# Optimization experiments

Hardware: AMD Instinct MI355X
Metric: run time of the kernel (lower is better)

Reference implementation:

```python
import jax, jax.numpy as jnp
import numpy as np

N, E, D = 50000, 1600000, 128


def _mk_w(key, shape):
    return jax.random.normal(key, shape, dtype=jnp.float32) * 0.05


def setup_inputs() -> dict:
    key = jax.random.key(0)
    ks = jax.random.split(key, 32)
    inp = {
        'x_in': jax.random.normal(ks[0], (N, D), dtype=jnp.float32),
        'rows': jax.random.randint(ks[1], (E,), 0, N, dtype=jnp.int64 if jax.config.jax_enable_x64 else jnp.int32),
        'cols': jax.random.randint(ks[2], (E,), 0, N, dtype=jnp.int64 if jax.config.jax_enable_x64 else jnp.int32),
        'vals': jax.random.uniform(ks[3], (E,), dtype=jnp.float32),
    }
    names = ['m1_W1', 'm1_W2', 'm2_W1', 'm2_W2', 'Wu1', 'Wu2', 'Wr1', 'Wr2', 'Wo1', 'Wo2']
    for i, n in enumerate(names):
        inp[n] = _mk_w(ks[4 + i], (D, D))
        inp[n.replace('W', 'b')] = jnp.zeros((D,), dtype=jnp.float32)
    return inp


def _mlp2(x, W1, b1, W2, b2):
    # 2-layer MLP: Linear -> ReLU -> Linear
    return jax.nn.relu(x @ W1 + b1) @ W2 + b2


def reference(x_in, rows, cols, vals,
              m1_W1, m1_b1, m1_W2, m1_b2,
              m2_W1, m2_b1, m2_W2, m2_b2,
              Wu1, bu1, Wu2, bu2,
              Wr1, br1, Wr2, br2,
              Wo1, bo1, Wo2, bo2):
    x = _mlp2(x_in, m1_W1, m1_b1, m1_W2, m1_b2)            # [N, D]
    # sparse COO spmm: out[i] = sum_e vals[e] * x[cols[e]] for rows[e] == i
    msgs = vals[:, None] * x[cols]                          # [E, D]
    agg = jax.ops.segment_sum(msgs, rows, num_segments=N)   # [N, D]
    out = _mlp2(agg, m2_W1, m2_b1, m2_W2, m2_b2)
    z = jax.nn.sigmoid(out @ Wu1 + bu1 + x @ Wu2 + bu2)
    r = jax.nn.sigmoid(out @ Wr1 + br1 + x @ Wr2 + br2)
    h = jnp.tanh(out @ Wo1 + bo1 + (r * x) @ Wo2 + bo2)
    return (1.0 - z) * x + z * h
```

## Files before the change

kernel.cpp:

```cpp
#include <hip/hip_runtime.h>

#define DD 128
#define BSHIFT 7
#define BROWS 128
#define MS_TILE 4096
#define MS_EPT 8
#define STAGE_CAP 6144

typedef __attribute__((ext_vector_type(8))) short short8;
typedef __attribute__((ext_vector_type(4))) float f32x4;
typedef unsigned short u16;
typedef unsigned int u32;

__device__ __forceinline__ u16 f2bf(float f) {
  u32 u = __builtin_bit_cast(u32, f);
  u += 0x7fffu + ((u >> 16) & 1u);
  return (u16)(u >> 16);
}
__device__ __forceinline__ float bf2f(u16 s) {
  u32 u = ((u32)s) << 16;
  return __builtin_bit_cast(float, u);
}
__device__ __forceinline__ float f16val(u32 cv) {
  return (float)__builtin_bit_cast(_Float16, (u16)(cv & 0xffffu));
}
__device__ __forceinline__ float sigmoidf_(float v) { return 1.f / (1.f + __expf(-v)); }
__device__ __forceinline__ float tanhf_(float v) {
  float e = __expf(-2.f * v);
  return (1.f - e) / (1.f + e);
}

struct WPtrs { const float* w[10]; };

__global__ void pack_weights(WPtrs wp, u16* __restrict__ bp) {
  const float* W = wp.w[blockIdx.x];
  u16* out = bp + (size_t)blockIdx.x * 16384;
  for (int o = threadIdx.x; o < 16384; o += blockDim.x) {
    int e = o & 7, lane = (o >> 3) & 63, nt = (o >> 9) & 7, ks = o >> 12;
    int k = ks * 32 + (lane >> 4) * 8 + e;
    int c = (lane & 15) + nt * 16;
    out[o] = f2bf(W[k * DD + c]);
  }
}

__global__ __launch_bounds__(512) void multisplit(const int* __restrict__ rows,
                                                  const int* __restrict__ cols,
                                                  const float* __restrict__ vals,
                                                  int* __restrict__ cursor,
                                                  uint2* __restrict__ recs,
                                                  int E, int NB, int cap) {
  __shared__ u32 hist[512];
  __shared__ u32 scan_tmp[512];
  __shared__ u32 hbase[512];
  __shared__ int gbase[512];
  __shared__ u32 rankc[512];
  __shared__ uint2 stage[MS_TILE];
  const int t = threadIdx.x;
  const int tile0 = blockIdx.x * MS_TILE;
  hist[t] = 0;
  rankc[t] = 0;
  __syncthreads();
  int myb[MS_EPT];
  u32 mycv[MS_EPT], myrow[MS_EPT];
#pragma unroll
  for (int j = 0; j < MS_EPT; ++j) {
    int e = tile0 + j * 512 + t;
    if (e < E) {
      int r = rows[e];
      int b = r >> BSHIFT;
      myb[j] = b;
      myrow[j] = (u32)r;
      _Float16 hf = (_Float16)vals[e];
      mycv[j] = ((u32)cols[e] << 16) | (u32)__builtin_bit_cast(u16, hf);
      atomicAdd(&hist[b], 1u);
    } else {
      myb[j] = -1;
    }
  }
  __syncthreads();
  u32 v = hist[t];
  scan_tmp[t] = v;
  __syncthreads();
  for (int o = 1; o < 512; o <<= 1) {
    u32 x = (t >= o) ? scan_tmp[t - o] : 0;
    __syncthreads();
    scan_tmp[t] += x;
    __syncthreads();
  }
  hbase[t] = scan_tmp[t] - v;
  if (t < NB && v > 0) gbase[t] = atomicAdd(&cursor[t], (int)v);
  __syncthreads();
#pragma unroll
  for (int j = 0; j < MS_EPT; ++j) {
    if (myb[j] >= 0) {
      u32 rk = atomicAdd(&rankc[myb[j]], 1u);
      stage[hbase[myb[j]] + rk].x = mycv[j];
      stage[hbase[myb[j]] + rk].y = myrow[j];
    }
  }
  __syncthreads();
  int cnt = E - tile0;
  cnt = cnt < MS_TILE ? cnt : MS_TILE;
  for (int k = t; k < cnt; k += 512) {
    uint2 rec = stage[k];
    int b = (int)(rec.y >> BSHIFT);
    int off = gbase[b] + (k - (int)hbase[b]);
    if (off < cap) recs[(size_t)b * cap + off] = rec;
  }
}

__global__ __launch_bounds__(512) void bucket_csr(const uint2* __restrict__ recs,
                                                  const int* __restrict__ cursor,
                                                  u32* __restrict__ recs2,
                                                  int* __restrict__ rowstart,
                                                  int* __restrict__ rowcnt, int n, int cap) {
  __shared__ int hist[BROWS];
  __shared__ int sc[BROWS];
  __shared__ int hbase[BROWS];
  __shared__ u32 rank[BROWS];
  __shared__ u32 stage[STAGE_CAP];
  const int t = threadIdx.x;
  const int b = blockIdx.x;
  int cnt = cursor[b];
  cnt = cnt < cap ? cnt : cap;
  const uint2* rb = recs + (size_t)b * cap;
  if (t < BROWS) { hist[t] = 0; rank[t] = 0; }
  __syncthreads();
  for (int i = t; i < cnt; i += 512) atomicAdd(&hist[rb[i].y & (BROWS - 1)], 1);
  __syncthreads();
  if (t < BROWS) sc[t] = hist[t];
  __syncthreads();
  for (int o = 1; o < BROWS; o <<= 1) {
    int x = (t >= o && t < BROWS) ? sc[t - o] : 0;
    __syncthreads();
    if (t < BROWS) sc[t] += x;
    __syncthreads();
  }
  if (t < BROWS) {
    hbase[t] = sc[t] - hist[t];
    int r = (b << BSHIFT) + t;
    if (r < n) {
      rowstart[r] = b * cap + hbase[t];
      rowcnt[r] = hist[t];
    }
  }
  __syncthreads();
  for (int i = t; i < cnt; i += 512) {
    uint2 rec = rb[i];
    int lr = (int)(rec.y & (BROWS - 1));
    u32 p = atomicAdd(&rank[lr], 1u);
    stage[hbase[lr] + p] = rec.x;
  }
  __syncthreads();
  u32* ob = recs2 + (size_t)b * cap;
  for (int i = t; i < cnt; i += 512) ob[i] = stage[i];
}

__global__ void spmm_agg(const int* __restrict__ rowstart, const int* __restrict__ rowcnt,
                         const u32* __restrict__ recs2, const u16* __restrict__ xb,
                         u16* __restrict__ aggb, int n) {
  int row = blockIdx.x * 4 + (threadIdx.x >> 6);
  int lane = threadIdx.x & 63;
  if (row >= n) return;
  const int s = rowstart[row];
  const int cnt = rowcnt[row];
  const int hi = lane >> 5;
  const int l32 = lane & 31;
  float a0 = 0.f, a1 = 0.f, a2 = 0.f, a3 = 0.f;
  int j = 0;
#define SPMM_PAIR(P)                                                                   \
  {                                                                                    \
    u32 pk0 = recs2[s + j + 2 * (P)];                                                  \
    u32 pk1 = recs2[s + j + 2 * (P) + 1];                                              \
    u32 pk = hi ? pk1 : pk0;                                                           \
    uint2 xv = *(reinterpret_cast<const uint2*>(xb + (size_t)(pk >> 16) * DD) + l32);  \
    float vv = f16val(pk);                                                             \
    a0 += vv * bf2f((u16)(xv.x & 0xffffu));                                            \
    a1 += vv * bf2f((u16)(xv.x >> 16));                                                \
    a2 += vv * bf2f((u16)(xv.y & 0xffffu));                                            \
    a3 += vv * bf2f((u16)(xv.y >> 16));                                                \
  }
  for (; j + 15 < cnt; j += 16) {
    SPMM_PAIR(0) SPMM_PAIR(1) SPMM_PAIR(2) SPMM_PAIR(3)
    SPMM_PAIR(4) SPMM_PAIR(5) SPMM_PAIR(6) SPMM_PAIR(7)
  }
  for (; j + 1 < cnt; j += 2) { SPMM_PAIR(0) }
  if (j < cnt) {
    u32 pk0 = recs2[s + j];
    uint2 xv = *(reinterpret_cast<const uint2*>(xb + (size_t)(pk0 >> 16) * DD) + l32);
    float vv = hi ? 0.f : f16val(pk0);
    a0 += vv * bf2f((u16)(xv.x & 0xffffu));
    a1 += vv * bf2f((u16)(xv.x >> 16));
    a2 += vv * bf2f((u16)(xv.y & 0xffffu));
    a3 += vv * bf2f((u16)(xv.y >> 16));
  }
#undef SPMM_PAIR
  a0 += __shfl_xor(a0, 32, 64);
  a1 += __shfl_xor(a1, 32, 64);
  a2 += __shfl_xor(a2, 32, 64);
  a3 += __shfl_xor(a3, 32, 64);
  if (!hi) {
    uint2 o;
    o.x = ((u32)f2bf(a1) << 16) | (u32)f2bf(a0);
    o.y = ((u32)f2bf(a3) << 16) | (u32)f2bf(a2);
    *reinterpret_cast<uint2*>(aggb + (size_t)row * DD + l32 * 4) = o;
  }
}

template <int ASRC>
__global__ __launch_bounds__(256) void mlp_fused(const void* __restrict__ Ain,
                                                 const u16* __restrict__ W1p,
                                                 const float* __restrict__ b1,
                                                 const u16* __restrict__ W2p,
                                                 const float* __restrict__ b2,
                                                 u16* __restrict__ outB, int n) {
  __shared__ u16 sm[32][136];
  const int lane = threadIdx.x & 63;
  const int wid = threadIdx.x >> 6;
  const int m = wid >> 1, c = wid & 1;
  const int row0 = blockIdx.x * 32 + m * 16;
  const int ar = lane & 15, ak = (lane >> 4) * 8;
  const int crow = 4 * (lane >> 4), ccol = lane & 15;

  f32x4 acc[4];
#pragma unroll
  for (int t = 0; t < 4; ++t) acc[t] = f32x4{0.f, 0.f, 0.f, 0.f};

#pragma unroll
  for (int ks = 0; ks < 4; ++ks) {
    short8 a;
    int r = row0 + ar;
    r = r < n ? r : n - 1;
    if (ASRC == 0) {
      const float* Ap = (const float*)Ain + (size_t)r * DD + ks * 32 + ak;
      float4 f0 = *reinterpret_cast<const float4*>(Ap);
      float4 f1 = *reinterpret_cast<const float4*>(Ap + 4);
      short8 tv;
      tv[0] = (short)f2bf(f0.x); tv[1] = (short)f2bf(f0.y);
      tv[2] = (short)f2bf(f0.z); tv[3] = (short)f2bf(f0.w);
      tv[4] = (short)f2bf(f1.x); tv[5] = (short)f2bf(f1.y);
      tv[6] = (short)f2bf(f1.z); tv[7] = (short)f2bf(f1.w);
      a = tv;
    } else {
      a = *reinterpret_cast<const short8*>((const u16*)Ain + (size_t)r * DD + ks * 32 + ak);
    }
#pragma unroll
    for (int nt4 = 0; nt4 < 4; ++nt4) {
      int nt = c * 4 + nt4;
      short8 bfr = *reinterpret_cast<const short8*>(W1p + (((ks * 8 + nt) * 64 + lane) * 8));
      acc[nt4] = __builtin_amdgcn_mfma_f32_16x16x32_bf16(a, bfr, acc[nt4], 0, 0, 0);
    }
  }
#pragma unroll
  for (int nt4 = 0; nt4 < 4; ++nt4) {
    int col = (c * 4 + nt4) * 16 + ccol;
    float bsv = b1[col];
#pragma unroll
    for (int e = 0; e < 4; ++e) {
      float v = acc[nt4][e] + bsv;
      v = v > 0.f ? v : 0.f;
      sm[m * 16 + crow + e][col] = f2bf(v);
    }
  }
  __syncthreads();

  f32x4 acc2[4];
#pragma unroll
  for (int t = 0; t < 4; ++t) acc2[t] = f32x4{0.f, 0.f, 0.f, 0.f};
#pragma unroll
  for (int ks = 0; ks < 4; ++ks) {
    short8 a2 = *reinterpret_cast<const short8*>(&sm[m * 16 + ar][ks * 32 + ak]);
#pragma unroll
    for (int nt4 = 0; nt4 < 4; ++nt4) {
      int nt = c * 4 + nt4;
      short8 bfr = *reinterpret_cast<const short8*>(W2p + (((ks * 8 + nt) * 64 + lane) * 8));
      acc2[nt4] = __builtin_amdgcn_mfma_f32_16x16x32_bf16(a2, bfr, acc2[nt4], 0, 0, 0);
    }
  }
#pragma unroll
  for (int nt4 = 0; nt4 < 4; ++nt4) {
    int col = (c * 4 + nt4) * 16 + ccol;
    float bsv = b2[col];
#pragma unroll
    for (int e = 0; e < 4; ++e) {
      int r = row0 + crow + e;
      if (r < n) outB[(size_t)r * DD + col] = f2bf(acc2[nt4][e] + bsv);
    }
  }
}

__global__ __launch_bounds__(256) void mlp2_gates_final(
    const u16* __restrict__ Agg, const u16* __restrict__ Ax, const u16* __restrict__ W3p,
    const float* __restrict__ b3, const u16* __restrict__ W4p, const float* __restrict__ b4,
    const u16* __restrict__ Wu1p, const u16* __restrict__ Wu2p, const u16* __restrict__ Wr1p,
    const u16* __restrict__ Wr2p, const u16* __restrict__ Wo1p, const u16* __restrict__ Wo2p,
    const float* __restrict__ bu1, const float* __restrict__ bu2, const float* __restrict__ br1,
    const float* __restrict__ br2, const float* __restrict__ bo1, const float* __restrict__ bo2,
    float* __restrict__ out, int n) {
  __shared__ u16 sm[32][136];
  const int lane = threadIdx.x & 63;
  const int wid = threadIdx.x >> 6;
  const int m = wid >> 1, c = wid & 1;
  const int row0 = blockIdx.x * 32 + m * 16;
  const int ar = lane & 15, ak = (lane >> 4) * 8;
  const int crow = 4 * (lane >> 4), ccol = lane & 15;

  f32x4 acc[4];
#pragma unroll
  for (int t = 0; t < 4; ++t) acc[t] = f32x4{0.f, 0.f, 0.f, 0.f};
#pragma unroll
  for (int ks = 0; ks < 4; ++ks) {
    int r = row0 + ar;
    r = r < n ? r : n - 1;
    short8 a = *reinterpret_cast<const short8*>(Agg + (size_t)r * DD + ks * 32 + ak);
#pragma unroll
    for (int nt4 = 0; nt4 < 4; ++nt4) {
      int nt = c * 4 + nt4;
      short8 bfr = *reinterpret_cast<const short8*>(W3p + (((ks * 8 + nt) * 64 + lane) * 8));
      acc[nt4] = __builtin_amdgcn_mfma_f32_16x16x32_bf16(a, bfr, acc[nt4], 0, 0, 0);
    }
  }
#pragma unroll
  for (int nt4 = 0; nt4 < 4; ++nt4) {
    int col = (c * 4 + nt4) * 16 + ccol;
    float bsv = b3[col];
#pragma unroll
    for (int e = 0; e < 4; ++e) {
      float v = acc[nt4][e] + bsv;
      v = v > 0.f ? v : 0.f;
      sm[m * 16 + crow + e][col] = f2bf(v);
    }
  }
  __syncthreads();

#pragma unroll
  for (int t = 0; t < 4; ++t) acc[t] = f32x4{0.f, 0.f, 0.f, 0.f};
#pragma unroll
  for (int ks = 0; ks < 4; ++ks) {
    short8 a2 = *reinterpret_cast<const short8*>(&sm[m * 16 + ar][ks * 32 + ak]);
#pragma unroll
    for (int nt4 = 0; nt4 < 4; ++nt4) {
      int nt = c * 4 + nt4;
      short8 bfr = *reinterpret_cast<const short8*>(W4p + (((ks * 8 + nt) * 64 + lane) * 8));
      acc[nt4] = __builtin_amdgcn_mfma_f32_16x16x32_bf16(a2, bfr, acc[nt4], 0, 0, 0);
    }
  }
  __syncthreads();
#pragma unroll
  for (int nt4 = 0; nt4 < 4; ++nt4) {
    int col = (c * 4 + nt4) * 16 + ccol;
    float bsv = b4[col];
#pragma unroll
    for (int e = 0; e < 4; ++e)
      sm[m * 16 + crow + e][col] = f2bf(acc[nt4][e] + bsv);
  }
  __syncthreads();

  f32x4 aZ[4], aR[4], aO[4];
#pragma unroll
  for (int t = 0; t < 4; ++t) {
    aZ[t] = f32x4{0.f, 0.f, 0.f, 0.f};
    aR[t] = f32x4{0.f, 0.f, 0.f, 0.f};
    aO[t] = f32x4{0.f, 0.f, 0.f, 0.f};
  }
#pragma unroll
  for (int ks = 0; ks < 4; ++ks) {
    int r = row0 + ar;
    r = r < n ? r : n - 1;
    short8 ao = *reinterpret_cast<const short8*>(&sm[m * 16 + ar][ks * 32 + ak]);
    short8 ax = *reinterpret_cast<const short8*>(Ax + (size_t)r * DD + ks * 32 + ak);
#pragma unroll
    for (int nt4 = 0; nt4 < 4; ++nt4) {
      int nt = c * 4 + nt4;
      size_t bo = (size_t)(((ks * 8 + nt) * 64 + lane) * 8);
      short8 b1 = *reinterpret_cast<const short8*>(Wu1p + bo);
      short8 b2 = *reinterpret_cast<const short8*>(Wu2p + bo);
      short8 b3f = *reinterpret_cast<const short8*>(Wr1p + bo);
      short8 b4f = *reinterpret_cast<const short8*>(Wr2p + bo);
      short8 b5 = *reinterpret_cast<const short8*>(Wo1p + bo);
      aZ[nt4] = __builtin_amdgcn_mfma_f32_16x16x32_bf16(ao, b1, aZ[nt4], 0, 0, 0);
      aZ[nt4] = __builtin_amdgcn_mfma_f32_16x16x32_bf16(ax, b2, aZ[nt4], 0, 0, 0);
      aR[nt4] = __builtin_amdgcn_mfma_f32_16x16x32_bf16(ao, b3f, aR[nt4], 0, 0, 0);
      aR[nt4] = __builtin_amdgcn_mfma_f32_16x16x32_bf16(ax, b4f, aR[nt4], 0, 0, 0);
      aO[nt4] = __builtin_amdgcn_mfma_f32_16x16x32_bf16(ao, b5, aO[nt4], 0, 0, 0);
    }
  }
  __syncthreads();
#pragma unroll
  for (int nt4 = 0; nt4 < 4; ++nt4) {
    int col = (c * 4 + nt4) * 16 + ccol;
    float bz = bu1[col] + bu2[col];
    float br_ = br1[col] + br2[col];
    float bo_ = bo1[col];
#pragma unroll
    for (int e = 0; e < 4; ++e) {
      int r = row0 + crow + e;
      float z = sigmoidf_(aZ[nt4][e] + bz);
      float rr = sigmoidf_(aR[nt4][e] + br_);
      aZ[nt4][e] = z;
      aO[nt4][e] = aO[nt4][e] + bo_;
      float xv = 0.f;
      if (r < n) xv = bf2f(Ax[(size_t)r * DD + col]);
      sm[m * 16 + crow + e][col] = f2bf(rr * xv);
    }
  }
  __syncthreads();

  f32x4 acc2[4];
#pragma unroll
  for (int t = 0; t < 4; ++t) acc2[t] = f32x4{0.f, 0.f, 0.f, 0.f};
#pragma unroll
  for (int ks = 0; ks < 4; ++ks) {
    short8 a2 = *reinterpret_cast<const short8*>(&sm[m * 16 + ar][ks * 32 + ak]);
#pragma unroll
    for (int nt4 = 0; nt4 < 4; ++nt4) {
      int nt = c * 4 + nt4;
      short8 bfr = *reinterpret_cast<const short8*>(Wo2p + (((ks * 8 + nt) * 64 + lane) * 8));
      acc2[nt4] = __builtin_amdgcn_mfma_f32_16x16x32_bf16(a2, bfr, acc2[nt4], 0, 0, 0);
    }
  }
#pragma unroll
  for (int nt4 = 0; nt4 < 4; ++nt4) {
    int col = (c * 4 + nt4) * 16 + ccol;
    float bo2v = bo2[col];
#pragma unroll
    for (int e = 0; e < 4; ++e) {
      int r = row0 + crow + e;
      if (r < n) {
        size_t idx = (size_t)r * DD + col;
        float oi = acc2[nt4][e] + bo2v + aO[nt4][e];
        float h = tanhf_(oi);
        float z = aZ[nt4][e];
        float xv = bf2f(Ax[idx]);
        out[idx] = (1.f - z) * xv + z * h;
      }
    }
  }
}

extern "C" void kernel_launch(void* const* d_in, const int* in_sizes, int n_in,
                              void* d_out, int out_size, void* d_ws, size_t ws_size,
                              hipStream_t stream) {
  const int n = in_sizes[0] / DD;
  const int E = in_sizes[1];
  const float* x_in = (const float*)d_in[0];
  const int* rows = (const int*)d_in[1];
  const int* cols = (const int*)d_in[2];
  const float* vals = (const float*)d_in[3];
  const float* Wm[10];
  const float* Bm[10];
  for (int i = 0; i < 10; ++i) {
    Wm[i] = (const float*)d_in[4 + 2 * i];
    Bm[i] = (const float*)d_in[5 + 2 * i];
  }

  const int NB = (n + BROWS - 1) >> BSHIFT;
  int cap = (((E / NB) * 5) / 4 + 511) & ~511;
  cap = cap < STAGE_CAP ? cap : STAGE_CAP;

  char* base = (char*)d_ws;
  size_t off = 0;
  auto alloc = [&](size_t bytes) -> char* {
    char* p = base + off;
    off += (bytes + 255) & ~(size_t)255;
    return p;
  };
  u16* wpack = (u16*)alloc((size_t)10 * 16384 * 2);
  u16* x_b = (u16*)alloc((size_t)n * DD * 2);
  u16* agg_b = (u16*)alloc((size_t)n * DD * 2);
  int* cursor = (int*)alloc((size_t)NB * 4);
  int* rowstart = (int*)alloc((size_t)n * 4);
  int* rowcnt = (int*)alloc((size_t)n * 4);
  uint2* recs = (uint2*)alloc((size_t)NB * cap * 8);
  u32* recs2 = (u32*)alloc((size_t)NB * cap * 4);
  (void)ws_size;
  (void)n_in;
  (void)out_size;

  hipMemsetAsync(cursor, 0, (size_t)NB * 4, stream);
  WPtrs wp;
  for (int i = 0; i < 10; ++i) wp.w[i] = Wm[i];
  pack_weights<<<10, 256, 0, stream>>>(wp, wpack);
  multisplit<<<(E + MS_TILE - 1) / MS_TILE, 512, 0, stream>>>(rows, cols, vals, cursor, recs, E,
                                                             NB, cap);
  bucket_csr<<<NB, 512, 0, stream>>>(recs, cursor, recs2, rowstart, rowcnt, n, cap);
  int gblocks = (n + 31) / 32;
  mlp_fused<0><<<gblocks, 256, 0, stream>>>(x_in, wpack + 0 * 16384, Bm[0], wpack + 1 * 16384,
                                            Bm[1], x_b, n);
  spmm_agg<<<(n + 3) / 4, 256, 0, stream>>>(rowstart, rowcnt, recs2, x_b, agg_b, n);
  mlp2_gates_final<<<gblocks, 256, 0, stream>>>(
      agg_b, x_b, wpack + 2 * 16384, Bm[2], wpack + 3 * 16384, Bm[3], wpack + 4 * 16384,
      wpack + 5 * 16384, wpack + 6 * 16384, wpack + 7 * 16384, wpack + 8 * 16384,
      wpack + 9 * 16384, Bm[4], Bm[5], Bm[6], Bm[7], Bm[8], Bm[9], (float*)d_out, n);
}
```

Measured before the change: 287.8 us.

## Fold m2 second linear into gate weights and co-launch multisplit with first MLP

Precomposes m2_W2 with Wu1, Wr1 and Wo1 (and the matching biases) in a small compose kernel. The final kernel then skips one 128x128 GEMM stage and one LDS round trip per tile. It also merges the edge multisplit and the first MLP into one heterogeneous launch, with blocks picking their role by index, so the two independent stages overlap on the GPU. The costs are an extra tiny compose launch, weights now composed in fp32 and then rounded to bf16 (which changes rounding), and larger LDS usage in the merged kernel.

```diff
diff --git a/kernel.cpp b/kernel.cpp
--- a/kernel.cpp
+++ b/kernel.cpp
@@ -6,6 +6,7 @@
 #define MS_TILE 4096
 #define MS_EPT 8
 #define STAGE_CAP 6144
+#define MSB_LDS 43008
 
 typedef __attribute__((ext_vector_type(8))) short short8;
 typedef __attribute__((ext_vector_type(4))) float f32x4;
@@ -31,6 +32,38 @@
 }
 
 struct WPtrs { const float* w[10]; };
+
+__global__ __launch_bounds__(256) void compose(const float* __restrict__ W4,
+                                               const float* __restrict__ Wu1,
+                                               const float* __restrict__ Wr1,
+                                               const float* __restrict__ Wo1,
+                                               const float* __restrict__ b4,
+                                               const float* __restrict__ bu1,
+                                               const float* __restrict__ bu2,
+                                               const float* __restrict__ br1,
+                                               const float* __restrict__ br2,
+                                               const float* __restrict__ bo1,
+                                               float* __restrict__ Wc, float* __restrict__ bc) {
+  const int mat = blockIdx.x >> 3;
+  const int rowg = blockIdx.x & 7;
+  const float* Ws = (mat == 0) ? Wu1 : (mat == 1) ? Wr1 : Wo1;
+  float* out = Wc + (size_t)mat * 16384;
+  for (int i = threadIdx.x; i < 2048; i += 256) {
+    int k = rowg * 16 + (i >> 7);
+    int c = i & 127;
+    float s = 0.f;
+#pragma unroll 8
+    for (int j = 0; j < 128; ++j) s += W4[k * 128 + j] * Ws[j * 128 + c];
+    out[k * 128 + c] = s;
+  }
+  if (rowg == 0 && threadIdx.x < 128) {
+    int c = threadIdx.x;
+    float s = 0.f;
+    for (int k = 0; k < 128; ++k) s += b4[k] * Ws[k * 128 + c];
+    float base = (mat == 0) ? (bu1[c] + bu2[c]) : (mat == 1) ? (br1[c] + br2[c]) : bo1[c];
+    bc[mat * 128 + c] = base + s;
+  }
+}
 
 __global__ void pack_weights(WPtrs wp, u16* __restrict__ bp) {
   const float* W = wp.w[blockIdx.x];
@@ -43,69 +76,138 @@
   }
 }
 
-__global__ __launch_bounds__(512) void multisplit(const int* __restrict__ rows,
-                                                  const int* __restrict__ cols,
-                                                  const float* __restrict__ vals,
-                                                  int* __restrict__ cursor,
-                                                  uint2* __restrict__ recs,
-                                                  int E, int NB, int cap) {
-  __shared__ u32 hist[512];
-  __shared__ u32 scan_tmp[512];
-  __shared__ u32 hbase[512];
-  __shared__ int gbase[512];
-  __shared__ u32 rankc[512];
-  __shared__ uint2 stage[MS_TILE];
+__global__ __launch_bounds__(512) void ms_mlp_fused(
+    const int* __restrict__ rows, const int* __restrict__ cols, const float* __restrict__ vals,
+    int* __restrict__ cursor, uint2* __restrict__ recs, int E, int NB, int cap, int msBlocks,
+    const float* __restrict__ Ain, const u16* __restrict__ W1p, const float* __restrict__ b1,
+    const u16* __restrict__ W2p, const float* __restrict__ b2, u16* __restrict__ outB, int n) {
+  __shared__ __align__(16) char smraw[MSB_LDS];
   const int t = threadIdx.x;
-  const int tile0 = blockIdx.x * MS_TILE;
-  hist[t] = 0;
-  rankc[t] = 0;
-  __syncthreads();
-  int myb[MS_EPT];
-  u32 mycv[MS_EPT], myrow[MS_EPT];
-#pragma unroll
-  for (int j = 0; j < MS_EPT; ++j) {
-    int e = tile0 + j * 512 + t;
-    if (e < E) {
-      int r = rows[e];
-      int b = r >> BSHIFT;
-      myb[j] = b;
-      myrow[j] = (u32)r;
-      _Float16 hf = (_Float16)vals[e];
-      mycv[j] = ((u32)cols[e] << 16) | (u32)__builtin_bit_cast(u16, hf);
-      atomicAdd(&hist[b], 1u);
-    } else {
-      myb[j] = -1;
-    }
-  }
-  __syncthreads();
-  u32 v = hist[t];
-  scan_tmp[t] = v;
-  __syncthreads();
-  for (int o = 1; o < 512; o <<= 1) {
-    u32 x = (t >= o) ? scan_tmp[t - o] : 0;
-    __syncthreads();
-    scan_tmp[t] += x;
-    __syncthreads();
-  }
-  hbase[t] = scan_tmp[t] - v;
-  if (t < NB && v > 0) gbase[t] = atomicAdd(&cursor[t], (int)v);
-  __syncthreads();
-#pragma unroll
-  for (int j = 0; j < MS_EPT; ++j) {
-    if (myb[j] >= 0) {
-      u32 rk = atomicAdd(&rankc[myb[j]], 1u);
-      stage[hbase[myb[j]] + rk].x = mycv[j];
-      stage[hbase[myb[j]] + rk].y = myrow[j];
-    }
-  }
-  __syncthreads();
-  int cnt = E - tile0;
-  cnt = cnt < MS_TILE ? cnt : MS_TILE;
-  for (int k = t; k < cnt; k += 512) {
-    uint2 rec = stage[k];
-    int b = (int)(rec.y >> BSHIFT);
-    int off = gbase[b] + (k - (int)hbase[b]);
-    if (off < cap) recs[(size_t)b * cap + off] = rec;
+  if (blockIdx.x < msBlocks) {
+    u32* hist = (u32*)smraw;
+    u32* scan_tmp = (u32*)(smraw + 2048);
+    u32* hbase = (u32*)(smraw + 4096);
+    int* gbase = (int*)(smraw + 6144);
+    u32* rankc = (u32*)(smraw + 8192);
+    uint2* stage = (uint2*)(smraw + 10240);
+    const int tile0 = blockIdx.x * MS_TILE;
+    hist[t] = 0;
+    rankc[t] = 0;
+    __syncthreads();
+    int myb[MS_EPT];
+    u32 mycv[MS_EPT], myrow[MS_EPT];
+#pragma unroll
+    for (int j = 0; j < MS_EPT; ++j) {
+      int e = tile0 + j * 512 + t;
+      if (e < E) {
+        int r = rows[e];
+        int b = r >> BSHIFT;
+        myb[j] = b;
+        myrow[j] = (u32)r;
+        _Float16 hf = (_Float16)vals[e];
+        mycv[j] = ((u32)cols[e] << 16) | (u32)__builtin_bit_cast(u16, hf);
+        atomicAdd(&hist[b], 1u);
+      } else {
+        myb[j] = -1;
+      }
+    }
+    __syncthreads();
+    u32 v = hist[t];
+    scan_tmp[t] = v;
+    __syncthreads();
+    for (int o = 1; o < 512; o <<= 1) {
+      u32 x = (t >= o) ? scan_tmp[t - o] : 0;
+      __syncthreads();
+      scan_tmp[t] += x;
+      __syncthreads();
+    }
+    hbase[t] = scan_tmp[t] - v;
+    if (t < NB && v > 0) gbase[t] = atomicAdd(&cursor[t], (int)v);
+    __syncthreads();
+#pragma unroll
+    for (int j = 0; j < MS_EPT; ++j) {
+      if (myb[j] >= 0) {
+        u32 rk = atomicAdd(&rankc[myb[j]], 1u);
+        stage[hbase[myb[j]] + rk].x = mycv[j];
+        stage[hbase[myb[j]] + rk].y = myrow[j];
+      }
+    }
+    __syncthreads();
+    int cnt = E - tile0;
+    cnt = cnt < MS_TILE ? cnt : MS_TILE;
+    for (int k = t; k < cnt; k += 512) {
+      uint2 rec = stage[k];
+      int b = (int)(rec.y >> BSHIFT);
+      int off = gbase[b] + (k - (int)hbase[b]);
+      if (off < cap) recs[(size_t)b * cap + off] = rec;
+    }
+  } else {
+    u16(*sm)[136] = (u16(*)[136])smraw;
+    const int lane = t & 63;
+    const int wid = t >> 6;
+    const int tile = wid >> 1;
+    const int c = wid & 1;
+    const int row0 = (blockIdx.x - msBlocks) * 64 + tile * 16;
+    const int ar = lane & 15, ak = (lane >> 4) * 8;
+    const int crow = 4 * (lane >> 4), ccol = lane & 15;
+
+    f32x4 acc[4];
+#pragma unroll
+    for (int q = 0; q < 4; ++q) acc[q] = f32x4{0.f, 0.f, 0.f, 0.f};
+#pragma unroll
+    for (int ks = 0; ks < 4; ++ks) {
+      int r = row0 + ar;
+      r = r < n ? r : n - 1;
+      const float* Ap = Ain + (size_t)r * DD + ks * 32 + ak;
+      float4 f0 = *reinterpret_cast<const float4*>(Ap);
+      float4 f1 = *reinterpret_cast<const float4*>(Ap + 4);
+      short8 a;
+      a[0] = (short)f2bf(f0.x); a[1] = (short)f2bf(f0.y);
+      a[2] = (short)f2bf(f0.z); a[3] = (short)f2bf(f0.w);
+      a[4] = (short)f2bf(f1.x); a[5] = (short)f2bf(f1.y);
+      a[6] = (short)f2bf(f1.z); a[7] = (short)f2bf(f1.w);
+#pragma unroll
+      for (int nt4 = 0; nt4 < 4; ++nt4) {
+        int nt = c * 4 + nt4;
+        short8 bfr = *reinterpret_cast<const short8*>(W1p + (((ks * 8 + nt) * 64 + lane) * 8));
+        acc[nt4] = __builtin_amdgcn_mfma_f32_16x16x32_bf16(a, bfr, acc[nt4], 0, 0, 0);
+      }
+    }
+#pragma unroll
+    for (int nt4 = 0; nt4 < 4; ++nt4) {
+      int col = (c * 4 + nt4) * 16 + ccol;
+      float bsv = b1[col];
+#pragma unroll
+      for (int e = 0; e < 4; ++e) {
+        float v = acc[nt4][e] + bsv;
+        v = v > 0.f ? v : 0.f;
+        sm[tile * 16 + crow + e][col] = f2bf(v);
+      }
+    }
+    __syncthreads();
+    f32x4 acc2[4];
+#pragma unroll
+    for (int q = 0; q < 4; ++q) acc2[q] = f32x4{0.f, 0.f, 0.f, 0.f};
+#pragma unroll
+    for (int ks = 0; ks < 4; ++ks) {
+      short8 a2 = *reinterpret_cast<const short8*>(&sm[tile * 16 + ar][ks * 32 + ak]);
+#pragma unroll
+      for (int nt4 = 0; nt4 < 4; ++nt4) {
+        int nt = c * 4 + nt4;
+        short8 bfr = *reinterpret_cast<const short8*>(W2p + (((ks * 8 + nt) * 64 + lane) * 8));
+        acc2[nt4] = __builtin_amdgcn_mfma_f32_16x16x32_bf16(a2, bfr, acc2[nt4], 0, 0, 0);
+      }
+    }
+#pragma unroll
+    for (int nt4 = 0; nt4 < 4; ++nt4) {
+      int col = (c * 4 + nt4) * 16 + ccol;
+      float bsv = b2[col];
+#pragma unroll
+      for (int e = 0; e < 4; ++e) {
+        int r = row0 + crow + e;
+        if (r < n) outB[(size_t)r * DD + col] = f2bf(acc2[nt4][e] + bsv);
+      }
+    }
   }
 }
 
@@ -207,13 +309,13 @@
   }
 }
 
-template <int ASRC>
-__global__ __launch_bounds__(256) void mlp_fused(const void* __restrict__ Ain,
-                                                 const u16* __restrict__ W1p,
-                                                 const float* __restrict__ b1,
-                                                 const u16* __restrict__ W2p,
-                                                 const float* __restrict__ b2,
-                                                 u16* __restrict__ outB, int n) {
+__global__ __launch_bounds__(256) void gates_final2(
+    const u16* __restrict__ Agg, const u16* __restrict__ Ax, const u16* __restrict__ W3p,
+    const float* __restrict__ b3, const u16* __restrict__ Wu1p, const u16* __restrict__ Wu2p,
+    const u16* __restrict__ Wr1p, const u16* __restrict__ Wr2p, const u16* __restrict__ Wo1p,
+    const u16* __restrict__ Wo2p, const float* __restrict__ bzc, const float* __restrict__ brc,
+    const float* __restrict__ boc, const float* __restrict__ bo2, float* __restrict__ out,
+    int n) {
   __shared__ u16 sm[32][136];
   const int lane = threadIdx.x & 63;
   const int wid = threadIdx.x >> 6;
@@ -224,37 +326,23 @@
 
   f32x4 acc[4];
 #pragma unroll
-  for (int t = 0; t < 4; ++t) acc[t] = f32x4{0.f, 0.f, 0.f, 0.f};
-
+  for (int q = 0; q < 4; ++q) acc[q] = f32x4{0.f, 0.f, 0.f, 0.f};
 #pragma unroll
   for (int ks = 0; ks < 4; ++ks) {
-    short8 a;
     int r = row0 + ar;
     r = r < n ? r : n - 1;
-    if (ASRC == 0) {
-      const float* Ap = (const float*)Ain + (size_t)r * DD + ks * 32 + ak;
-      float4 f0 = *reinterpret_cast<const float4*>(Ap);
-      float4 f1 = *reinterpret_cast<const float4*>(Ap + 4);
-      short8 tv;
-      tv[0] = (short)f2bf(f0.x); tv[1] = (short)f2bf(f0.y);
-      tv[2] = (short)f2bf(f0.z); tv[3] = (short)f2bf(f0.w);
-      tv[4] = (short)f2bf(f1.x); tv[5] = (short)f2bf(f1.y);
-      tv[6] = (short)f2bf(f1.z); tv[7] = (short)f2bf(f1.w);
-      a = tv;
-    } else {
-      a = *reinterpret_cast<const short8*>((const u16*)Ain + (size_t)r * DD + ks * 32 + ak);
-    }
+    short8 a = *reinterpret_cast<const short8*>(Agg + (size_t)r * DD + ks * 32 + ak);
 #pragma unroll
     for (int nt4 = 0; nt4 < 4; ++nt4) {
       int nt = c * 4 + nt4;
-      short8 bfr = *reinterpret_cast<const short8*>(W1p + (((ks * 8 + nt) * 64 + lane) * 8));
+      short8 bfr = *reinterpret_cast<const short8*>(W3p + (((ks * 8 + nt) * 64 + lane) * 8));
       acc[nt4] = __builtin_amdgcn_mfma_f32_16x16x32_bf16(a, bfr, acc[nt4], 0, 0, 0);
     }
   }
 #pragma unroll
   for (int nt4 = 0; nt4 < 4; ++nt4) {
     int col = (c * 4 + nt4) * 16 + ccol;
-    float bsv = b1[col];
+    float bsv = b3[col];
 #pragma unroll
     for (int e = 0; e < 4; ++e) {
       float v = acc[nt4][e] + bsv;
@@ -264,104 +352,12 @@
   }
   __syncthreads();
 
-  f32x4 acc2[4];
-#pragma unroll
-  for (int t = 0; t < 4; ++t) acc2[t] = f32x4{0.f, 0.f, 0.f, 0.f};
-#pragma unroll
-  for (int ks = 0; ks < 4; ++ks) {
-    short8 a2 = *reinterpret_cast<const short8*>(&sm[m * 16 + ar][ks * 32 + ak]);
-#pragma unroll
-    for (int nt4 = 0; nt4 < 4; ++nt4) {
-      int nt = c * 4 + nt4;
-      short8 bfr = *reinterpret_cast<const short8*>(W2p + (((ks * 8 + nt) * 64 + lane) * 8));
-      acc2[nt4] = __builtin_amdgcn_mfma_f32_16x16x32_bf16(a2, bfr, acc2[nt4], 0, 0, 0);
-    }
-  }
-#pragma unroll
-  for (int nt4 = 0; nt4 < 4; ++nt4) {
-    int col = (c * 4 + nt4) * 16 + ccol;
-    float bsv = b2[col];
-#pragma unroll
-    for (int e = 0; e < 4; ++e) {
-      int r = row0 + crow + e;
-      if (r < n) outB[(size_t)r * DD + col] = f2bf(acc2[nt4][e] + bsv);
-    }
-  }
-}
-
-__global__ __launch_bounds__(256) void mlp2_gates_final(
-    const u16* __restrict__ Agg, const u16* __restrict__ Ax, const u16* __restrict__ W3p,
-    const float* __restrict__ b3, const u16* __restrict__ W4p, const float* __restrict__ b4,
-    const u16* __restrict__ Wu1p, const u16* __restrict__ Wu2p, const u16* __restrict__ Wr1p,
-    const u16* __restrict__ Wr2p, const u16* __restrict__ Wo1p, const u16* __restrict__ Wo2p,
-    const float* __restrict__ bu1, const float* __restrict__ bu2, const float* __restrict__ br1,
-    const float* __restrict__ br2, const float* __restrict__ bo1, const float* __restrict__ bo2,
-    float* __restrict__ out, int n) {
-  __shared__ u16 sm[32][136];
-  const int lane = threadIdx.x & 63;
-  const int wid = threadIdx.x >> 6;
-  const int m = wid >> 1, c = wid & 1;
-  const int row0 = blockIdx.x * 32 + m * 16;
-  const int ar = lane & 15, ak = (lane >> 4) * 8;
-  const int crow = 4 * (lane >> 4), ccol = lane & 15;
-
-  f32x4 acc[4];
-#pragma unroll
-  for (int t = 0; t < 4; ++t) acc[t] = f32x4{0.f, 0.f, 0.f, 0.f};
-#pragma unroll
-  for (int ks = 0; ks < 4; ++ks) {
-    int r = row0 + ar;
-    r = r < n ? r : n - 1;
-    short8 a = *reinterpret_cast<const short8*>(Agg + (size_t)r * DD + ks * 32 + ak);
-#pragma unroll
-    for (int nt4 = 0; nt4 < 4; ++nt4) {
-      int nt = c * 4 + nt4;
-      short8 bfr = *reinterpret_cast<const short8*>(W3p + (((ks * 8 + nt) * 64 + lane) * 8));
-      acc[nt4] = __builtin_amdgcn_mfma_f32_16x16x32_bf16(a, bfr, acc[nt4], 0, 0, 0);
-    }
-  }
-#pragma unroll
-  for (int nt4 = 0; nt4 < 4; ++nt4) {
-    int col = (c * 4 + nt4) * 16 + ccol;
-    float bsv = b3[col];
-#pragma unroll
-    for (int e = 0; e < 4; ++e) {
-      float v = acc[nt4][e] + bsv;
-      v = v > 0.f ? v : 0.f;
-      sm[m * 16 + crow + e][col] = f2bf(v);
-    }
-  }
-  __syncthreads();
-
-#pragma unroll
-  for (int t = 0; t < 4; ++t) acc[t] = f32x4{0.f, 0.f, 0.f, 0.f};
-#pragma unroll
-  for (int ks = 0; ks < 4; ++ks) {
-    short8 a2 = *reinterpret_cast<const short8*>(&sm[m * 16 + ar][ks * 32 + ak]);
-#pragma unroll
-    for (int nt4 = 0; nt4 < 4; ++nt4) {
-      int nt = c * 4 + nt4;
-      short8 bfr = *reinterpret_cast<const short8*>(W4p + (((ks * 8 + nt) * 64 + lane) * 8));
-      acc[nt4] = __builtin_amdgcn_mfma_f32_16x16x32_bf16(a2, bfr, acc[nt4], 0, 0, 0);
-    }
-  }
-  __syncthreads();
-#pragma unroll
-  for (int nt4 = 0; nt4 < 4; ++nt4) {
-    int col = (c * 4 + nt4) * 16 + ccol;
-    float bsv = b4[col];
-#pragma unroll
-    for (int e = 0; e < 4; ++e)
-      sm[m * 16 + crow + e][col] = f2bf(acc[nt4][e] + bsv);
-  }
-  __syncthreads();
-
   f32x4 aZ[4], aR[4], aO[4];
 #pragma unroll
-  for (int t = 0; t < 4; ++t) {
-    aZ[t] = f32x4{0.f, 0.f, 0.f, 0.f};
-    aR[t] = f32x4{0.f, 0.f, 0.f, 0.f};
-    aO[t] = f32x4{0.f, 0.f, 0.f, 0.f};
+  for (int q = 0; q < 4; ++q) {
+    aZ[q] = f32x4{0.f, 0.f, 0.f, 0.f};
+    aR[q] = f32x4{0.f, 0.f, 0.f, 0.f};
+    aO[q] = f32x4{0.f, 0.f, 0.f, 0.f};
   }
 #pragma unroll
   for (int ks = 0; ks < 4; ++ks) {
@@ -389,9 +385,9 @@
 #pragma unroll
   for (int nt4 = 0; nt4 < 4; ++nt4) {
     int col = (c * 4 + nt4) * 16 + ccol;
-    float bz = bu1[col] + bu2[col];
-    float br_ = br1[col] + br2[col];
-    float bo_ = bo1[col];
+    float bz = bzc[col];
+    float br_ = brc[col];
+    float bo_ = boc[col];
 #pragma unroll
     for (int e = 0; e < 4; ++e) {
       int r = row0 + crow + e;
@@ -408,7 +404,7 @@
 
   f32x4 acc2[4];
 #pragma unroll
-  for (int t = 0; t < 4; ++t) acc2[t] = f32x4{0.f, 0.f, 0.f, 0.f};
+  for (int q = 0; q < 4; ++q) acc2[q] = f32x4{0.f, 0.f, 0.f, 0.f};
 #pragma unroll
   for (int ks = 0; ks < 4; ++ks) {
     short8 a2 = *reinterpret_cast<const short8*>(&sm[m * 16 + ar][ks * 32 + ak]);
@@ -465,7 +461,9 @@
     off += (bytes + 255) & ~(size_t)255;
     return p;
   };
-  u16* wpack = (u16*)alloc((size_t)10 * 16384 * 2);
+  u16* wpack = (u16*)alloc((size_t)9 * 16384 * 2);
+  float* Wc = (float*)alloc((size_t)3 * 16384 * 4);
+  float* bc = (float*)alloc((size_t)3 * 128 * 4);
   u16* x_b = (u16*)alloc((size_t)n * DD * 2);
   u16* agg_b = (u16*)alloc((size_t)n * DD * 2);
   int* cursor = (int*)alloc((size_t)NB * 4);
@@ -478,18 +476,23 @@
   (void)out_size;
 
   hipMemsetAsync(cursor, 0, (size_t)NB * 4, stream);
+  compose<<<24, 256, 0, stream>>>(Wm[3], Wm[4], Wm[6], Wm[8], Bm[3], Bm[4], Bm[5], Bm[6], Bm[7],
+                                  Bm[8], Wc, bc);
   WPtrs wp;
-  for (int i = 0; i < 10; ++i) wp.w[i] = Wm[i];
-  pack_weights<<<10, 256, 0, stream>>>(wp, wpack);
-  multisplit<<<(E + MS_TILE - 1) / MS_TILE, 512, 0, stream>>>(rows, cols, vals, cursor, recs, E,
-                                                             NB, cap);
+  wp.w[0] = Wm[0]; wp.w[1] = Wm[1]; wp.w[2] = Wm[2];
+  wp.w[3] = Wc + 0; wp.w[4] = Wm[5]; wp.w[5] = Wc + 16384;
+  wp.w[6] = Wm[7]; wp.w[7] = Wc + 32768; wp.w[8] = Wm[9];
+  wp.w[9] = Wm[9];
+  pack_weights<<<9, 256, 0, stream>>>(wp, wpack);
+  const int msB = (E + MS_TILE - 1) / MS_TILE;
+  const int mlpB = (n + 63) / 64;
+  ms_mlp_fused<<<msB + mlpB, 512, 0, stream>>>(rows, cols, vals, cursor, recs, E, NB, cap, msB,
+                                               x_in, wpack + 0 * 16384, Bm[0],
+                                               wpack + 1 * 16384, Bm[1], x_b, n);
   bucket_csr<<<NB, 512, 0, stream>>>(recs, cursor, recs2, rowstart, rowcnt, n, cap);
-  int gblocks = (n + 31) / 32;
-  mlp_fused<0><<<gblocks, 256, 0, stream>>>(x_in, wpack + 0 * 16384, Bm[0], wpack + 1 * 16384,
-                                            Bm[1], x_b, n);
   spmm_agg<<<(n + 3) / 4, 256, 0, stream>>>(rowstart, rowcnt, recs2, x_b, agg_b, n);
-  mlp2_gates_final<<<gblocks, 256, 0, stream>>>(
-      agg_b, x_b, wpack + 2 * 16384, Bm[2], wpack + 3 * 16384, Bm[3], wpack + 4 * 16384,
-      wpack + 5 * 16384, wpack + 6 * 16384, wpack + 7 * 16384, wpack + 8 * 16384,
-      wpack + 9 * 16384, Bm[4], Bm[5], Bm[6], Bm[7], Bm[8], Bm[9], (float*)d_out, n);
-}
+  gates_final2<<<(n + 31) / 32, 256, 0, stream>>>(
+      agg_b, x_b, wpack + 2 * 16384, Bm[2], wpack + 3 * 16384, wpack + 4 * 16384,
+      wpack + 5 * 16384, wpack + 6 * 16384, wpack + 7 * 16384, wpack + 8 * 16384, bc + 0,
+      bc + 128, bc + 256, Bm[9], (float*)d_out, n);
+}
```

New measurement: 315.6 us. 1.1x slower.
